# Optimization experiments

Measured on AMD Instinct MI355X. Metric: run time of the kernel, lower is better.

## Reference

```python
import jax, jax.numpy as jnp
import numpy as np

B, LC, LQ, D = 16, 1024, 128, 512


def setup_inputs() -> dict:
    key = jax.random.key(0)
    k1, k2, k3, k4, k5 = jax.random.split(key, 5)
    return {
        "C": jax.random.normal(k1, (B, LC, D), dtype=jnp.float32),
        "Q": jax.random.normal(k2, (B, LQ, D), dtype=jnp.float32),
        "Cmask": jax.random.randint(k3, (B, LC), 0, 2, dtype=jnp.int32),
        "Qmask": jax.random.randint(k4, (B, LQ), 0, 2, dtype=jnp.int32),
        "w_sim": jax.random.normal(k5, (3 * D,), dtype=jnp.float32) * (1.0 / np.sqrt(3 * D)),
    }


def reference(C, Q, Cmask, Qmask, w_sim):
    d = C.shape[-1]
    # Decompose Linear(3d -> 1) on cat([C_rep, Q_rep, C*Q]) into three dot products:
    # S[b,i,j] = C[b,i].w1 + Q[b,j].w2 + (C[b,i]*Q[b,j]).w3
    w1, w2, w3 = w_sim[:d], w_sim[d:2 * d], w_sim[2 * d:]
    s_c = C @ w1                                    # (B, Lc)
    s_q = Q @ w2                                    # (B, Lq)
    s_cq = jnp.einsum('bid,bjd->bij', C * w3, Q)    # (B, Lc, Lq)
    S = s_c[:, :, None] + s_q[:, None, :] + s_cq    # (B, Lc, Lq)

    NEG = jnp.asarray(-1e10, S.dtype)
    S1 = jax.nn.softmax(jnp.where(Qmask[:, None, :] != 0, NEG, S), axis=2)  # over question
    S2 = jax.nn.softmax(jnp.where(Cmask[:, :, None] != 0, NEG, S), axis=1)  # over context

    A = jnp.einsum('bij,bjd->bid', S1, Q)                       # (B, Lc, d)
    # bmm(bmm(S1, S2^T), C) == S1 @ (S2^T @ C) (associativity, avoids Lc x Lc)
    S2tC = jnp.einsum('bij,bid->bjd', S2, C)                    # (B, Lq, d)
    Bv = jnp.einsum('bij,bjd->bid', S1, S2tC)                   # (B, Lc, d)

    # dropout treated as identity (eval / p-effective 0) for the reference
    return jnp.concatenate([C, A, C * A, C * Bv], axis=2)       # (B, Lc, 4d)
```

## Files before the change

### kernel.cpp

```cpp
#include <hip/hip_runtime.h>
#include <hip/hip_bf16.h>
#include <math.h>

#define NB 16
#define NLC 1024
#define NLQ 128
#define ND 512
#define NEGV (-1.0e10f)

typedef __attribute__((ext_vector_type(8))) short bf16x8f;
typedef __attribute__((ext_vector_type(4))) float f32x4a;

__device__ inline unsigned short f2bf(float f) {
    unsigned u = __float_as_uint(f);
    unsigned r = (u + 0x7fffu + ((u >> 16) & 1u)) >> 16;
    return (unsigned short)r;
}

__device__ inline int xcd_swz(int bid, int nwg) {
    int chunk = nwg >> 3;
    return (bid & 7) * chunk + (bid >> 3);
}

__global__ __launch_bounds__(512) void k_prep2(const float* __restrict__ C,
                                               const float* __restrict__ Q,
                                               const float* __restrict__ w,
                                               unsigned short* __restrict__ Cw3,
                                               unsigned short* __restrict__ Ct,
                                               unsigned short* __restrict__ Qb,
                                               unsigned short* __restrict__ Qt,
                                               float* __restrict__ sc,
                                               float* __restrict__ sq) {
    __shared__ float T[64][65];
    int x = blockIdx.x, t = threadIdx.x;
    const float* src; const float* wdot; const float* wmul;
    unsigned short* rout; unsigned short* tout; float* sdst;
    int rows;
    if (x < 256) {
        int b = x >> 4, r0t = (x & 15) * 64;
        src = C + ((size_t)b * NLC + r0t) * ND;
        wdot = w; wmul = w + 2 * ND;
        rout = Cw3 + ((size_t)b * NLC + r0t) * ND;
        tout = Ct + (size_t)b * ND * NLC + r0t;
        sdst = sc + b * NLC + r0t;
        rows = NLC;
    } else {
        int x2 = x - 256;
        int b = x2 >> 1, r0t = (x2 & 1) * 64;
        src = Q + ((size_t)b * NLQ + r0t) * ND;
        wdot = w + ND; wmul = nullptr;
        rout = Qb + ((size_t)b * NLQ + r0t) * ND;
        tout = Qt + (size_t)b * ND * NLQ + r0t;
        sdst = sq + b * NLQ + r0t;
        rows = NLQ;
    }
    int r = t >> 3;
    int s8 = (t & 7) * 8;
    float dacc = 0.f;
    for (int c = 0; c < 8; ++c) {
        int dbase = c * 64 + s8;
        float4 v0 = *(const float4*)&src[(size_t)r * ND + dbase];
        float4 v1 = *(const float4*)&src[(size_t)r * ND + dbase + 4];
        float4 wd0 = *(const float4*)&wdot[dbase];
        float4 wd1 = *(const float4*)&wdot[dbase + 4];
        dacc += v0.x * wd0.x + v0.y * wd0.y + v0.z * wd0.z + v0.w * wd0.w;
        dacc += v1.x * wd1.x + v1.y * wd1.y + v1.z * wd1.z + v1.w * wd1.w;
        float f8[8] = {v0.x, v0.y, v0.z, v0.w, v1.x, v1.y, v1.z, v1.w};
        unsigned short o[8];
        if (wmul) {
            float4 w30 = *(const float4*)&wmul[dbase];
            float4 w31 = *(const float4*)&wmul[dbase + 4];
            float m8[8] = {w30.x, w30.y, w30.z, w30.w, w31.x, w31.y, w31.z, w31.w};
#pragma unroll
            for (int e = 0; e < 8; ++e) o[e] = f2bf(f8[e] * m8[e]);
        } else {
#pragma unroll
            for (int e = 0; e < 8; ++e) o[e] = f2bf(f8[e]);
        }
        *(int4*)&rout[(size_t)r * ND + dbase] = *(int4*)o;
#pragma unroll
        for (int e = 0; e < 8; ++e) T[r][s8 + e] = f8[e];
        __syncthreads();
        {
            int dd = t >> 3, seg = (t & 7) * 8;
            unsigned short o16[8];
#pragma unroll
            for (int e = 0; e < 8; ++e) o16[e] = f2bf(T[seg + e][dd]);
            *(int4*)&tout[(size_t)(c * 64 + dd) * rows + seg] = *(int4*)o16;
        }
        __syncthreads();
    }
    dacc += __shfl_xor(dacc, 1, 64);
    dacc += __shfl_xor(dacc, 2, 64);
    dacc += __shfl_xor(dacc, 4, 64);
    if ((t & 7) == 0) sdst[r] = dacc;
}

__global__ __launch_bounds__(256) void k_S(const unsigned short* __restrict__ Cw3,
                                           const unsigned short* __restrict__ Qb,
                                           const float* __restrict__ sc,
                                           const float* __restrict__ sq,
                                           const int* __restrict__ Qmask,
                                           const int* __restrict__ Cmask,
                                           unsigned short* __restrict__ P1,
                                           unsigned short* __restrict__ Eb,
                                           float* __restrict__ colm,
                                           float* __restrict__ cols) {
    __shared__ __align__(16) char lds[25088];
    int lg = xcd_swz(blockIdx.x, 256);
    int b = lg >> 4, it = lg & 15, i0 = it * 64;
    int t = threadIdx.x, lane = t & 63, wv = t >> 6;
    int g = lane >> 4, r16 = lane & 15;
    const unsigned short* Asrc = Cw3 + ((size_t)b * NLC + i0) * ND;
    const unsigned short* Bsrc = Qb + (size_t)b * NLQ * ND;
    f32x4a zero = {0.f, 0.f, 0.f, 0.f};
    f32x4a acc[8];
#pragma unroll
    for (int nf = 0; nf < 8; ++nf) acc[nf] = zero;

    for (int kk = 0; kk < 8; ++kk) {
#pragma unroll
        for (int p = 0; p < 2; ++p) {
            int u = t + p * 256;
            int i = u >> 3, db = u & 7;
            int4 v = *(const int4*)(Asrc + (size_t)i * ND + kk * 64 + db * 8);
            *(int4*)(lds + i * 128 + ((db * 16) ^ ((i & 7) << 4))) = v;
        }
#pragma unroll
        for (int p = 0; p < 4; ++p) {
            int u = t + p * 256;
            int j = u >> 3, db = u & 7;
            int4 v = *(const int4*)(Bsrc + (size_t)j * ND + kk * 64 + db * 8);
            *(int4*)(lds + 8192 + j * 128 + ((db * 16) ^ ((j & 7) << 4))) = v;
        }
        __syncthreads();
#pragma unroll
        for (int ks = 0; ks < 2; ++ks) {
            int inner = ks * 64 + g * 16;
            bf16x8f a = *(const bf16x8f*)(lds + (16 * wv + r16) * 128 + (inner ^ ((r16 & 7) << 4)));
#pragma unroll
            for (int nf = 0; nf < 8; ++nf) {
                bf16x8f bq = *(const bf16x8f*)(lds + 8192 + (16 * nf + r16) * 128 + (inner ^ ((r16 & 7) << 4)));
                acc[nf] = __builtin_amdgcn_mfma_f32_16x16x32_bf16(a, bq, acc[nf], 0, 0, 0);
            }
        }
        __syncthreads();
    }

    const float* scp = sc + b * NLC + i0;
    const float* sqp = sq + b * NLQ;
    const int* qm = Qmask + b * NLQ;
    const int* cmb = Cmask + b * NLC;
    float sv[8][4];
    float scr[4];
#pragma unroll
    for (int reg = 0; reg < 4; ++reg) scr[reg] = scp[16 * wv + 4 * g + reg];
    int qmv[8];
#pragma unroll
    for (int nf = 0; nf < 8; ++nf) {
        qmv[nf] = qm[16 * nf + r16];
        float sqv = sqp[16 * nf + r16];
#pragma unroll
        for (int reg = 0; reg < 4; ++reg) sv[nf][reg] = acc[nf][reg] + scr[reg] + sqv;
    }

    unsigned short* P1p = P1 + ((size_t)b * NLC + i0) * NLQ;
#pragma unroll
    for (int reg = 0; reg < 4; ++reg) {
        float m = -INFINITY;
#pragma unroll
        for (int nf = 0; nf < 8; ++nf) m = fmaxf(m, qmv[nf] ? NEGV : sv[nf][reg]);
#pragma unroll
        for (int off = 8; off >= 1; off >>= 1) m = fmaxf(m, __shfl_xor(m, off, 64));
        float pv[8], s = 0.f;
#pragma unroll
        for (int nf = 0; nf < 8; ++nf) {
            pv[nf] = __expf((qmv[nf] ? NEGV : sv[nf][reg]) - m);
            s += pv[nf];
        }
#pragma unroll
        for (int off = 8; off >= 1; off >>= 1) s += __shfl_xor(s, off, 64);
        float rsi = 1.0f / s;
        int i = 16 * wv + 4 * g + reg;
#pragma unroll
        for (int nf = 0; nf < 8; ++nf)
            P1p[(size_t)i * NLQ + 16 * nf + r16] = f2bf(pv[nf] * rsi);
    }

    int cmv[4];
#pragma unroll
    for (int reg = 0; reg < 4; ++reg) cmv[reg] = cmb[i0 + 16 * wv + 4 * g + reg];
    float vm2[8][4];
#pragma unroll
    for (int nf = 0; nf < 8; ++nf)
#pragma unroll
        for (int reg = 0; reg < 4; ++reg) vm2[nf][reg] = cmv[reg] ? NEGV : sv[nf][reg];

    float* cpm = (float*)(lds + 20480);
    float* cps = (float*)(lds + 22528);
    float* mtl = (float*)(lds + 24576);
    float cm8[8], cs8[8];
#pragma unroll
    for (int nf = 0; nf < 8; ++nf) {
        float m = vm2[nf][0];
#pragma unroll
        for (int reg = 1; reg < 4; ++reg) m = fmaxf(m, vm2[nf][reg]);
        float s = 0.f;
#pragma unroll
        for (int reg = 0; reg < 4; ++reg) s += __expf(vm2[nf][reg] - m);
#pragma unroll
        for (int off = 16; off <= 32; off <<= 1) {
            float mo = __shfl_xor(m, off, 64);
            float so = __shfl_xor(s, off, 64);
            float mn = fmaxf(m, mo);
            s = s * __expf(m - mn) + so * __expf(mo - mn);
            m = mn;
        }
        cm8[nf] = m; cs8[nf] = s;
    }
    if (g == 0) {
#pragma unroll
        for (int nf = 0; nf < 8; ++nf) {
            cpm[(wv * 8 + nf) * 16 + r16] = cm8[nf];
            cps[(wv * 8 + nf) * 16 + r16] = cs8[nf];
        }
    }
    __syncthreads();
    if (t < 128) {
        int j = t, nf = j >> 4, rr = j & 15;
        float M = cpm[(0 * 8 + nf) * 16 + rr];
        float S = cps[(0 * 8 + nf) * 16 + rr];
#pragma unroll
        for (int w2 = 1; w2 < 4; ++w2) {
            float mo = cpm[(w2 * 8 + nf) * 16 + rr];
            float so = cps[(w2 * 8 + nf) * 16 + rr];
            float mn = fmaxf(M, mo);
            S = S * __expf(M - mn) + so * __expf(mo - mn);
            M = mn;
        }
        colm[((size_t)b * 16 + it) * NLQ + j] = M;
        cols[((size_t)b * 16 + it) * NLQ + j] = S;
        mtl[j] = M;
    }
    __syncthreads();

    unsigned short* ex = (unsigned short*)lds;
#pragma unroll
    for (int nf = 0; nf < 8; ++nf) {
        float mj = mtl[16 * nf + r16];
        unsigned short e4[4];
#pragma unroll
        for (int reg = 0; reg < 4; ++reg) e4[reg] = f2bf(__expf(vm2[nf][reg] - mj));
        *(uint2*)&ex[(16 * nf + r16) * 80 + 16 * wv + 4 * g] = *(uint2*)e4;
    }
    __syncthreads();
    {
        int j = t >> 1, half = t & 1;
        unsigned short* Ep = Eb + ((size_t)b * NLQ + j) * NLC + i0 + half * 32;
#pragma unroll
        for (int c = 0; c < 4; ++c)
            *(int4*)&Ep[c * 8] = *(int4*)&ex[j * 80 + half * 32 + c * 8];
    }
}

__global__ __launch_bounds__(256) void k_s2tc(const unsigned short* __restrict__ Eb,
                                              const unsigned short* __restrict__ Ct,
                                              const float* __restrict__ colm,
                                              const float* __restrict__ cols,
                                              unsigned short* __restrict__ Vt) {
    __shared__ __align__(16) char lds[23552];
    int lg = xcd_swz(blockIdx.x, 128);
    int b = lg >> 3, dt = lg & 7;
    int t = threadIdx.x, lane = t & 63, wv = t >> 6, g = lane >> 4, r16 = lane & 15;
    float* fb = (float*)lds;

    if (t < 128) {
        int j = t;
        const float* cmp = colm + (size_t)b * 16 * NLQ + j;
        const float* csp = cols + (size_t)b * 16 * NLQ + j;
        float M = -INFINITY;
#pragma unroll
        for (int p = 0; p < 16; ++p) M = fmaxf(M, cmp[p * NLQ]);
        float S = 0.f;
#pragma unroll
        for (int p = 0; p < 16; ++p) S += csp[p * NLQ] * __expf(cmp[p * NLQ] - M);
        float inv = 1.0f / S;
#pragma unroll
        for (int p = 0; p < 16; ++p) fb[p * NLQ + j] = __expf(cmp[p * NLQ] - M) * inv;
    }

    const unsigned short* Ebb = Eb + (size_t)b * NLQ * NLC;
    const unsigned short* Ctb = Ct + ((size_t)b * ND + dt * 64) * NLC;
    int ja0 = t >> 2, ca0 = (t & 3) * 8;
    int ja1 = (t + 256) >> 2, ca1 = ((t + 256) & 3) * 8;
    int db0 = t >> 2, cb0 = (t & 3) * 8;

    f32x4a zero = {0.f, 0.f, 0.f, 0.f};
    f32x4a acc2[2][4], V[2][4];
#pragma unroll
    for (int mf = 0; mf < 2; ++mf)
#pragma unroll
        for (int nf = 0; nf < 4; ++nf) { acc2[mf][nf] = zero; V[mf][nf] = zero; }

    int4 ra0 = *(const int4*)(Ebb + (size_t)ja0 * NLC + ca0);
    int4 ra1 = *(const int4*)(Ebb + (size_t)ja1 * NLC + ca1);
    int4 rb  = *(const int4*)(Ctb + (size_t)db0 * NLC + cb0);
    __syncthreads();

    for (int ib = 0; ib < NLC; ib += 32) {
        *(int4*)(lds + 8192 + (ja0 * 40 + ca0) * 2) = ra0;
        *(int4*)(lds + 8192 + (ja1 * 40 + ca1) * 2) = ra1;
        *(int4*)(lds + 18432 + (db0 * 40 + cb0) * 2) = rb;
        __syncthreads();
        if (ib + 32 < NLC) {
            ra0 = *(const int4*)(Ebb + (size_t)ja0 * NLC + ib + 32 + ca0);
            ra1 = *(const int4*)(Ebb + (size_t)ja1 * NLC + ib + 32 + ca1);
            rb  = *(const int4*)(Ctb + (size_t)db0 * NLC + ib + 32 + cb0);
        }
#pragma unroll
        for (int mf = 0; mf < 2; ++mf) {
            bf16x8f a = *(const bf16x8f*)(lds + 8192 + ((32 * wv + 16 * mf + r16) * 40 + g * 8) * 2);
#pragma unroll
            for (int nf = 0; nf < 4; ++nf) {
                bf16x8f bb = *(const bf16x8f*)(lds + 18432 + ((16 * nf + r16) * 40 + g * 8) * 2);
                acc2[mf][nf] = __builtin_amdgcn_mfma_f32_16x16x32_bf16(a, bb, acc2[mf][nf], 0, 0, 0);
            }
        }
        __syncthreads();
        if (ib & 32) {
            int itg = ib >> 6;
#pragma unroll
            for (int mf = 0; mf < 2; ++mf) {
                f32x4a f4 = *(const f32x4a*)(lds + (itg * NLQ + 32 * wv + 16 * mf + 4 * g) * 4);
#pragma unroll
                for (int nf = 0; nf < 4; ++nf) {
#pragma unroll
                    for (int reg = 0; reg < 4; ++reg)
                        V[mf][nf][reg] += f4[reg] * acc2[mf][nf][reg];
                    acc2[mf][nf] = zero;
                }
            }
        }
    }
    unsigned short* vb = Vt + ((size_t)b * ND + dt * 64) * NLQ;
#pragma unroll
    for (int mf = 0; mf < 2; ++mf)
#pragma unroll
        for (int nf = 0; nf < 4; ++nf) {
            unsigned short o[4];
#pragma unroll
            for (int reg = 0; reg < 4; ++reg) o[reg] = f2bf(V[mf][nf][reg]);
            *(uint2*)&vb[(size_t)(16 * nf + r16) * NLQ + 32 * wv + 16 * mf + 4 * g] = *(uint2*)o;
        }
}

__global__ __launch_bounds__(256) void k_out(const unsigned short* __restrict__ P1,
                                             const unsigned short* __restrict__ Qt,
                                             const unsigned short* __restrict__ Vt,
                                             const float* __restrict__ C,
                                             float* __restrict__ Out) {
    __shared__ __align__(16) char lds[49152];
    int lg = xcd_swz(blockIdx.x, 2048);
    int b = lg >> 7, rem = lg & 127, it = rem >> 3, dt = rem & 7;
    int i0 = it * 64, d0 = dt * 64;
    int t = threadIdx.x, lane = t & 63, wv = t >> 6, g = lane >> 4, r16 = lane & 15;
    const unsigned short* P1b = P1 + ((size_t)b * NLC + i0) * NLQ;
    const unsigned short* Qtb = Qt + ((size_t)b * ND + d0) * NLQ;
    const unsigned short* Vtb = Vt + ((size_t)b * ND + d0) * NLQ;
#pragma unroll
    for (int p = 0; p < 4; ++p) {
        int u = t + p * 256;
        int r = u >> 4, c = u & 15;
        int swz = (c * 16) ^ ((r & 7) << 4);
        *(int4*)(lds + r * 256 + swz) = *(const int4*)(P1b + (size_t)r * NLQ + c * 8);
        *(int4*)(lds + 16384 + r * 256 + swz) = *(const int4*)(Qtb + (size_t)r * NLQ + c * 8);
        *(int4*)(lds + 32768 + r * 256 + swz) = *(const int4*)(Vtb + (size_t)r * NLQ + c * 8);
    }
    __syncthreads();
    f32x4a zero = {0.f, 0.f, 0.f, 0.f};
    f32x4a accA[4], accB[4];
#pragma unroll
    for (int nf = 0; nf < 4; ++nf) { accA[nf] = zero; accB[nf] = zero; }
#pragma unroll
    for (int ks = 0; ks < 4; ++ks) {
        int inner = ks * 64 + g * 16;
        bf16x8f a = *(const bf16x8f*)(lds + (16 * wv + r16) * 256 + (inner ^ ((r16 & 7) << 4)));
#pragma unroll
        for (int nf = 0; nf < 4; ++nf) {
            int ro = (16 * nf + r16) * 256 + (inner ^ ((r16 & 7) << 4));
            bf16x8f q = *(const bf16x8f*)(lds + 16384 + ro);
            accA[nf] = __builtin_amdgcn_mfma_f32_16x16x32_bf16(a, q, accA[nf], 0, 0, 0);
            bf16x8f vv = *(const bf16x8f*)(lds + 32768 + ro);
            accB[nf] = __builtin_amdgcn_mfma_f32_16x16x32_bf16(a, vv, accB[nf], 0, 0, 0);
        }
    }
    __syncthreads();

    float* At = (float*)lds;
    float* Bt = (float*)(lds + 17408);
#pragma unroll
    for (int nf = 0; nf < 4; ++nf) {
        int dloc = 16 * nf + r16;
#pragma unroll
        for (int reg = 0; reg < 4; ++reg) {
            int iloc = 16 * wv + 4 * g + reg;
            At[iloc * 68 + dloc] = accA[nf][reg];
            Bt[iloc * 68 + dloc] = accB[nf][reg];
        }
    }
    __syncthreads();

    const float* Cb = C + ((size_t)b * NLC + i0) * ND + d0;
    float* Ob = Out + ((size_t)b * NLC + i0) * (4 * ND);
#pragma unroll
    for (int p = 0; p < 4; ++p) {
        int u = t + p * 256;
        int row = u >> 4, c4 = (u & 15) * 4;
        float4 cv = *(const float4*)&Cb[(size_t)row * ND + c4];
        float4 av = *(const float4*)&At[row * 68 + c4];
        float4 bv = *(const float4*)&Bt[row * 68 + c4];
        float4 ca, cb;
        ca.x = cv.x * av.x; ca.y = cv.y * av.y; ca.z = cv.z * av.z; ca.w = cv.w * av.w;
        cb.x = cv.x * bv.x; cb.y = cv.y * bv.y; cb.z = cv.z * bv.z; cb.w = cv.w * bv.w;
        float* orow = Ob + (size_t)row * (4 * ND);
        *(float4*)&orow[d0 + c4] = cv;
        *(float4*)&orow[ND + d0 + c4] = av;
        *(float4*)&orow[2 * ND + d0 + c4] = ca;
        *(float4*)&orow[3 * ND + d0 + c4] = cb;
    }
}

extern "C" void kernel_launch(void* const* d_in, const int* in_sizes, int n_in,
                              void* d_out, int out_size, void* d_ws, size_t ws_size,
                              hipStream_t stream) {
    const float* C = (const float*)d_in[0];
    const float* Q = (const float*)d_in[1];
    const int* Cmask = (const int*)d_in[2];
    const int* Qmask = (const int*)d_in[3];
    const float* w = (const float*)d_in[4];
    float* out = (float*)d_out;

    char* ob = (char*)d_out;
    unsigned short* Cw3 = (unsigned short*)(ob + 0);
    unsigned short* Ct  = (unsigned short*)(ob + 16777216);
    unsigned short* Eb  = (unsigned short*)(ob + 33554432);
    unsigned short* Qb  = (unsigned short*)(ob + 37748736);
    float*          colm = (float*)(ob + 39845888);
    float*          colsv = (float*)(ob + 39976960);

    char* wb = (char*)d_ws;
    float* sc = (float*)(wb + 0);
    float* sq = (float*)(wb + 65536);
    unsigned short* P1 = (unsigned short*)(wb + 73728);
    unsigned short* Qt = (unsigned short*)(wb + 4268032);
    unsigned short* Vt = (unsigned short*)(wb + 6365184);

    k_prep2<<<dim3(288), dim3(512), 0, stream>>>(C, Q, w, Cw3, Ct, Qb, Qt, sc, sq);
    k_S<<<dim3(256), dim3(256), 0, stream>>>(Cw3, Qb, sc, sq, Qmask, Cmask, P1, Eb, colm, colsv);
    k_s2tc<<<dim3(128), dim3(256), 0, stream>>>(Eb, Ct, colm, colsv, Vt);
    k_out<<<dim3(2048), dim3(256), 0, stream>>>(P1, Qt, Vt, C, out);
}
```

Measured before the change: 80.51 us.

## Double grid sizes for prep and S2tC kernels with retiled K-step

k_prep2 now uses 32-row tiles with 256 threads, so 576 blocks are launched instead of 288. k_s2tc now splits D into 32-wide tiles, giving 256 blocks instead of 128. Its K step grows from 32 to 64 so each column-softmax scaling group is one loop iteration. The goal is to fill more of the GPU's compute units in these under-occupied kernels, at the cost of re-reading the E matrix twice as often in k_s2tc and issuing less MFMA work per block.

```diff
diff --git a/kernel.cpp b/kernel.cpp
--- a/kernel.cpp
+++ b/kernel.cpp
@@ -22,7 +22,7 @@
     return (bid & 7) * chunk + (bid >> 3);
 }
 
-__global__ __launch_bounds__(512) void k_prep2(const float* __restrict__ C,
+__global__ __launch_bounds__(256) void k_prep2(const float* __restrict__ C,
                                                const float* __restrict__ Q,
                                                const float* __restrict__ w,
                                                unsigned short* __restrict__ Cw3,
@@ -31,13 +31,13 @@
                                                unsigned short* __restrict__ Qt,
                                                float* __restrict__ sc,
                                                float* __restrict__ sq) {
-    __shared__ float T[64][65];
+    __shared__ float T[32][65];
     int x = blockIdx.x, t = threadIdx.x;
     const float* src; const float* wdot; const float* wmul;
     unsigned short* rout; unsigned short* tout; float* sdst;
     int rows;
-    if (x < 256) {
-        int b = x >> 4, r0t = (x & 15) * 64;
+    if (x < 512) {
+        int b = x >> 5, r0t = (x & 31) * 32;
         src = C + ((size_t)b * NLC + r0t) * ND;
         wdot = w; wmul = w + 2 * ND;
         rout = Cw3 + ((size_t)b * NLC + r0t) * ND;
@@ -45,8 +45,8 @@
         sdst = sc + b * NLC + r0t;
         rows = NLC;
     } else {
-        int x2 = x - 256;
-        int b = x2 >> 1, r0t = (x2 & 1) * 64;
+        int xq = x - 512;
+        int b = xq >> 2, r0t = (xq & 3) * 32;
         src = Q + ((size_t)b * NLQ + r0t) * ND;
         wdot = w + ND; wmul = nullptr;
         rout = Qb + ((size_t)b * NLQ + r0t) * ND;
@@ -82,7 +82,7 @@
         for (int e = 0; e < 8; ++e) T[r][s8 + e] = f8[e];
         __syncthreads();
         {
-            int dd = t >> 3, seg = (t & 7) * 8;
+            int dd = t >> 2, seg = (t & 3) * 8;
             unsigned short o16[8];
 #pragma unroll
             for (int e = 0; e < 8; ++e) o16[e] = f2bf(T[seg + e][dd]);
@@ -268,9 +268,9 @@
                                               const float* __restrict__ colm,
                                               const float* __restrict__ cols,
                                               unsigned short* __restrict__ Vt) {
-    __shared__ __align__(16) char lds[23552];
-    int lg = xcd_swz(blockIdx.x, 128);
-    int b = lg >> 3, dt = lg & 7;
+    __shared__ __align__(16) char lds[31232];
+    int lg = xcd_swz(blockIdx.x, 256);
+    int b = lg >> 4, dt = lg & 15;
     int t = threadIdx.x, lane = t & 63, wv = t >> 6, g = lane >> 4, r16 = lane & 15;
     float* fb = (float*)lds;
 
@@ -290,63 +290,71 @@
     }
 
     const unsigned short* Ebb = Eb + (size_t)b * NLQ * NLC;
-    const unsigned short* Ctb = Ct + ((size_t)b * ND + dt * 64) * NLC;
-    int ja0 = t >> 2, ca0 = (t & 3) * 8;
-    int ja1 = (t + 256) >> 2, ca1 = ((t + 256) & 3) * 8;
-    int db0 = t >> 2, cb0 = (t & 3) * 8;
+    const unsigned short* Ctb = Ct + ((size_t)b * ND + dt * 32) * NLC;
+    int ja0 = t >> 3, ca = (t & 7) * 8;
+    int db0 = t >> 3, cb = (t & 7) * 8;
 
     f32x4a zero = {0.f, 0.f, 0.f, 0.f};
-    f32x4a acc2[2][4], V[2][4];
+    f32x4a V[2][2];
 #pragma unroll
     for (int mf = 0; mf < 2; ++mf)
 #pragma unroll
-        for (int nf = 0; nf < 4; ++nf) { acc2[mf][nf] = zero; V[mf][nf] = zero; }
-
-    int4 ra0 = *(const int4*)(Ebb + (size_t)ja0 * NLC + ca0);
-    int4 ra1 = *(const int4*)(Ebb + (size_t)ja1 * NLC + ca1);
-    int4 rb  = *(const int4*)(Ctb + (size_t)db0 * NLC + cb0);
-    __syncthreads();
-
-    for (int ib = 0; ib < NLC; ib += 32) {
-        *(int4*)(lds + 8192 + (ja0 * 40 + ca0) * 2) = ra0;
-        *(int4*)(lds + 8192 + (ja1 * 40 + ca1) * 2) = ra1;
-        *(int4*)(lds + 18432 + (db0 * 40 + cb0) * 2) = rb;
-        __syncthreads();
-        if (ib + 32 < NLC) {
-            ra0 = *(const int4*)(Ebb + (size_t)ja0 * NLC + ib + 32 + ca0);
-            ra1 = *(const int4*)(Ebb + (size_t)ja1 * NLC + ib + 32 + ca1);
-            rb  = *(const int4*)(Ctb + (size_t)db0 * NLC + ib + 32 + cb0);
-        }
-#pragma unroll
-        for (int mf = 0; mf < 2; ++mf) {
-            bf16x8f a = *(const bf16x8f*)(lds + 8192 + ((32 * wv + 16 * mf + r16) * 40 + g * 8) * 2);
-#pragma unroll
-            for (int nf = 0; nf < 4; ++nf) {
-                bf16x8f bb = *(const bf16x8f*)(lds + 18432 + ((16 * nf + r16) * 40 + g * 8) * 2);
-                acc2[mf][nf] = __builtin_amdgcn_mfma_f32_16x16x32_bf16(a, bb, acc2[mf][nf], 0, 0, 0);
-            }
-        }
-        __syncthreads();
-        if (ib & 32) {
-            int itg = ib >> 6;
+        for (int nf = 0; nf < 2; ++nf) V[mf][nf] = zero;
+
+    int4 ra[4]; int4 rb;
+#pragma unroll
+    for (int p = 0; p < 4; ++p)
+        ra[p] = *(const int4*)(Ebb + (size_t)(ja0 + 32 * p) * NLC + ca);
+    rb = *(const int4*)(Ctb + (size_t)db0 * NLC + cb);
+    __syncthreads();
+
+    for (int ib = 0; ib < NLC; ib += 64) {
+#pragma unroll
+        for (int p = 0; p < 4; ++p)
+            *(int4*)(lds + 8192 + ((ja0 + 32 * p) * 72 + ca) * 2) = ra[p];
+        *(int4*)(lds + 26624 + (db0 * 72 + cb) * 2) = rb;
+        __syncthreads();
+        if (ib + 64 < NLC) {
+#pragma unroll
+            for (int p = 0; p < 4; ++p)
+                ra[p] = *(const int4*)(Ebb + (size_t)(ja0 + 32 * p) * NLC + ib + 64 + ca);
+            rb = *(const int4*)(Ctb + (size_t)db0 * NLC + ib + 64 + cb);
+        }
+        f32x4a acc2[2][2];
+#pragma unroll
+        for (int mf = 0; mf < 2; ++mf)
+#pragma unroll
+            for (int nf = 0; nf < 2; ++nf) acc2[mf][nf] = zero;
+#pragma unroll
+        for (int ks = 0; ks < 2; ++ks) {
+            int inner = ks * 32 + g * 8;
 #pragma unroll
             for (int mf = 0; mf < 2; ++mf) {
-                f32x4a f4 = *(const f32x4a*)(lds + (itg * NLQ + 32 * wv + 16 * mf + 4 * g) * 4);
-#pragma unroll
-                for (int nf = 0; nf < 4; ++nf) {
-#pragma unroll
-                    for (int reg = 0; reg < 4; ++reg)
-                        V[mf][nf][reg] += f4[reg] * acc2[mf][nf][reg];
-                    acc2[mf][nf] = zero;
+                bf16x8f a = *(const bf16x8f*)(lds + 8192 + ((32 * wv + 16 * mf + r16) * 72 + inner) * 2);
+#pragma unroll
+                for (int nf = 0; nf < 2; ++nf) {
+                    bf16x8f bb = *(const bf16x8f*)(lds + 26624 + ((16 * nf + r16) * 72 + inner) * 2);
+                    acc2[mf][nf] = __builtin_amdgcn_mfma_f32_16x16x32_bf16(a, bb, acc2[mf][nf], 0, 0, 0);
                 }
             }
         }
-    }
-    unsigned short* vb = Vt + ((size_t)b * ND + dt * 64) * NLQ;
+        __syncthreads();
+        int itg = ib >> 6;
+#pragma unroll
+        for (int mf = 0; mf < 2; ++mf) {
+            f32x4a f4 = *(const f32x4a*)(lds + (itg * NLQ + 32 * wv + 16 * mf + 4 * g) * 4);
+#pragma unroll
+            for (int nf = 0; nf < 2; ++nf)
+#pragma unroll
+                for (int reg = 0; reg < 4; ++reg)
+                    V[mf][nf][reg] += f4[reg] * acc2[mf][nf][reg];
+        }
+    }
+    unsigned short* vb = Vt + ((size_t)b * ND + dt * 32) * NLQ;
 #pragma unroll
     for (int mf = 0; mf < 2; ++mf)
 #pragma unroll
-        for (int nf = 0; nf < 4; ++nf) {
+        for (int nf = 0; nf < 2; ++nf) {
             unsigned short o[4];
 #pragma unroll
             for (int reg = 0; reg < 4; ++reg) o[reg] = f2bf(V[mf][nf][reg]);
@@ -455,8 +463,8 @@
     unsigned short* Qt = (unsigned short*)(wb + 4268032);
     unsigned short* Vt = (unsigned short*)(wb + 6365184);
 
-    k_prep2<<<dim3(288), dim3(512), 0, stream>>>(C, Q, w, Cw3, Ct, Qb, Qt, sc, sq);
+    k_prep2<<<dim3(576), dim3(256), 0, stream>>>(C, Q, w, Cw3, Ct, Qb, Qt, sc, sq);
     k_S<<<dim3(256), dim3(256), 0, stream>>>(Cw3, Qb, sc, sq, Qmask, Cmask, P1, Eb, colm, colsv);
-    k_s2tc<<<dim3(128), dim3(256), 0, stream>>>(Eb, Ct, colm, colsv, Vt);
+    k_s2tc<<<dim3(256), dim3(256), 0, stream>>>(Eb, Ct, colm, colsv, Vt);
     k_out<<<dim3(2048), dim3(256), 0, stream>>>(P1, Qt, Vt, C, out);
 }
```

Result: slower. 88.23 us (+9.6%).
